# Optimization experiments

Hardware: AMD Instinct MI355X
Metric: run time of the kernel (lower is better)

Reference implementation:

```python
import jax, jax.numpy as jnp
import numpy as np

N_NODES = 100000
N_EDGES = 1600000
K = 3


def _cheb_conv(x, row, col, w, W, b):
    # SpMM: out[row] += w * x[col]
    def spmm(v):
        return jax.ops.segment_sum(w[:, None] * v[col], row, num_segments=N_NODES)
    Ts = [x, spmm(x)]
    for _ in range(2, K):
        Ts.append(2.0 * spmm(Ts[-1]) - Ts[-2])
    return jnp.concatenate(Ts, axis=-1) @ W.T + b


def setup_inputs() -> dict:
    key = jax.random.key(0)
    ks = jax.random.split(key, 12)
    inp = {
        "x": jax.random.normal(ks[0], (N_NODES, 128), dtype=jnp.float32),
        "edge_index": jax.random.randint(ks[1], (2, N_EDGES), 0, N_NODES, dtype=jnp.int32),
        "edge_weight": jax.random.normal(ks[2], (N_EDGES,), dtype=jnp.float32) * 0.05,
        "W_in": jax.random.normal(ks[3], (128, K * 128), dtype=jnp.float32) * (1.0 / np.sqrt(K * 128)),
        "b_in": jnp.zeros((128,), dtype=jnp.float32),
        "W_h1": jax.random.normal(ks[4], (128, K * 128), dtype=jnp.float32) * (1.0 / np.sqrt(K * 128)),
        "b_h1": jnp.zeros((128,), dtype=jnp.float32),
        "W_h2": jax.random.normal(ks[5], (128, K * 128), dtype=jnp.float32) * (1.0 / np.sqrt(K * 128)),
        "b_h2": jnp.zeros((128,), dtype=jnp.float32),
        "W_out": jax.random.normal(ks[6], (64, K * 128), dtype=jnp.float32) * (1.0 / np.sqrt(K * 128)),
        "b_out": jnp.zeros((64,), dtype=jnp.float32),
    }
    return inp


def reference(x, edge_index, edge_weight, W_in, b_in, W_h1, b_h1, W_h2, b_h2, W_out, b_out):
    row, col = edge_index[0], edge_index[1]
    # dropout is inactive at inference (training=False)
    h = jax.nn.relu(_cheb_conv(x, row, col, edge_weight, W_in, b_in))
    for (W, b) in ((W_h1, b_h1), (W_h2, b_h2)):
        h = jax.nn.relu(_cheb_conv(h, row, col, edge_weight, W, b) + h)  # residual
    out = _cheb_conv(h, row, col, edge_weight, W_out, b_out)
    return out
```

## Files before the change

### kernel.cpp

```cpp
#include <hip/hip_runtime.h>
#include <hip/hip_bf16.h>
#include <stdint.h>
#include <stddef.h>

#define N_NODES 100000
#define N_EDGES 1600000
#define FEAT 128
#define NB_SCAN ((N_NODES + 255) / 256)
#define LDS_PITCH 136
#define CAP 24
#define NL (CAP / 4)
#define NBKT ((N_NODES + 255) / 256)
#define EPB 2048
#define NBLK ((N_EDGES + EPB - 1) / EPB)
#define EPT (EPB / 256)

typedef __attribute__((ext_vector_type(8))) short bf16x8;
typedef __attribute__((ext_vector_type(4))) float f32x4;
typedef unsigned short u16;

__device__ __forceinline__ float bf2f(u16 u) {
    union { unsigned int i; float f; } v; v.i = ((unsigned int)u) << 16; return v.f;
}
__device__ __forceinline__ u16 f2bf(float f) {
    union { float f; unsigned int i; } v; v.f = f;
    unsigned int x = v.i;
    return (u16)((x + 0x7fffu + ((x >> 16) & 1u)) >> 16);
}


__global__ void hist_kernel(const int* __restrict__ rows, int* __restrict__ counts) {
    int e = blockIdx.x * blockDim.x + threadIdx.x;
    if (e < N_EDGES) {
        int r = rows[e];
        r = min(max(r, 0), N_NODES - 1);
        atomicAdd(&counts[r], 1);
    }
}

__global__ void reduce_counts_kernel(const int* __restrict__ counts, int* __restrict__ bsum) {
    __shared__ int s[256];
    int i = blockIdx.x * 256 + threadIdx.x;
    int v = (i < N_NODES) ? counts[i] : 0;
    s[threadIdx.x] = v; __syncthreads();
    for (int off = 128; off > 0; off >>= 1) {
        if (threadIdx.x < off) s[threadIdx.x] += s[threadIdx.x + off];
        __syncthreads();
    }
    if (threadIdx.x == 0) bsum[blockIdx.x] = s[0];
}

__global__ void scan_bsums_kernel(int* __restrict__ bsum, int* __restrict__ row_ptr) {
    __shared__ int s[512];
    int t = threadIdx.x;
    int v = (t < NB_SCAN) ? bsum[t] : 0;
    s[t] = v; __syncthreads();
    for (int off = 1; off < 512; off <<= 1) {
        int x = (t >= off) ? s[t - off] : 0;
        __syncthreads();
        s[t] += x;
        __syncthreads();
    }
    if (t < NB_SCAN) bsum[t] = s[t] - v;
    if (t == NB_SCAN - 1) row_ptr[N_NODES] = s[t];
}

__global__ void write_rowptr_kernel(int* __restrict__ counts, const int* __restrict__ bsum,
                                    int* __restrict__ row_ptr) {
    __shared__ int s[256];
    int i = blockIdx.x * 256 + threadIdx.x;
    int v = (i < N_NODES) ? counts[i] : 0;
    s[threadIdx.x] = v; __syncthreads();
    for (int off = 1; off < 256; off <<= 1) {
        int x = (threadIdx.x >= off) ? s[threadIdx.x - off] : 0;
        __syncthreads();
        s[threadIdx.x] += x;
        __syncthreads();
    }
    if (i < N_NODES) {
        row_ptr[i] = bsum[blockIdx.x] + s[threadIdx.x] - v;
        counts[i] = 0;
    }
}

__global__ void scatter_kernel(const int* __restrict__ rows, const int* __restrict__ cols,
                               const float* __restrict__ w, const int* __restrict__ row_ptr,
                               int* __restrict__ fill, int2* __restrict__ ecw) {
    int e = blockIdx.x * blockDim.x + threadIdx.x;
    if (e < N_EDGES) {
        int r = rows[e];
        r = min(max(r, 0), N_NODES - 1);
        int pos = row_ptr[r] + atomicAdd(&fill[r], 1);
        pos = min(max(pos, 0), N_EDGES - 1);
        int c = cols[e];
        c = min(max(c, 0), N_NODES - 1);
        ecw[pos] = make_int2(c, __float_as_int(w[e]));
    }
}


__global__ __launch_bounds__(256) void csr_passA_kernel(const int* __restrict__ rows,
                                                        int* __restrict__ pcnt) {
    __shared__ int s_cnt[NBKT];
    int tid = threadIdx.x, blk = blockIdx.x;
    for (int b = tid; b < NBKT; b += 256) s_cnt[b] = 0;
    __syncthreads();
    int e0 = blk * EPB;
#pragma unroll
    for (int it = 0; it < EPT; ++it) {
        int e = e0 + it * 256 + tid;
        if (e < N_EDGES) {
            int r = min(max(rows[e], 0), N_NODES - 1);
            atomicAdd(&s_cnt[r >> 8], 1);
        }
    }
    __syncthreads();
    for (int b = tid; b < NBKT; b += 256)
        pcnt[(size_t)blk * NBKT + b] = s_cnt[b];
}

__global__ __launch_bounds__(256) void csr_scanP_kernel(int* __restrict__ pcnt,
                                                        int* __restrict__ gtot) {
    __shared__ int s[256];
    int b = blockIdx.x, tid = threadIdx.x;
    int carry = 0;
    for (int c = 0; c < (NBLK + 255) / 256; ++c) {
        int idx = c * 256 + tid;
        int v = (idx < NBLK) ? pcnt[(size_t)idx * NBKT + b] : 0;
        s[tid] = v; __syncthreads();
        for (int off = 1; off < 256; off <<= 1) {
            int x = (tid >= off) ? s[tid - off] : 0;
            __syncthreads();
            s[tid] += x;
            __syncthreads();
        }
        if (idx < NBLK) pcnt[(size_t)idx * NBKT + b] = carry + s[tid] - v;
        carry += s[255];
        __syncthreads();
    }
    if (tid == 0) gtot[b] = carry;
}

__global__ void csr_scanG_kernel(const int* __restrict__ gtot, int* __restrict__ bsum,
                                 int* __restrict__ row_ptr) {
    __shared__ int s[512];
    int t = threadIdx.x;
    int v = (t < NBKT) ? gtot[t] : 0;
    s[t] = v; __syncthreads();
    for (int off = 1; off < 512; off <<= 1) {
        int x = (t >= off) ? s[t - off] : 0;
        __syncthreads();
        s[t] += x;
        __syncthreads();
    }
    if (t < NBKT) bsum[t] = s[t] - v;
    if (t == NBKT - 1) {
        bsum[NBKT] = s[t];
        row_ptr[N_NODES] = s[t];
    }
}

__global__ __launch_bounds__(256) void csr_passB_kernel(const int* __restrict__ rows,
                                                        const int* __restrict__ cols,
                                                        const float* __restrict__ w,
                                                        const int* __restrict__ pcnt,
                                                        const int* __restrict__ bsum,
                                                        int2* __restrict__ ebuf) {
    __shared__ int s_base[NBKT];
    __shared__ int s_cnt[NBKT];
    __shared__ int s_off[NBKT];
    __shared__ int s_scan[512];
    __shared__ int2 s_sorted[EPB];
    __shared__ int s_dst[EPB];
    int tid = threadIdx.x, blk = blockIdx.x;
    for (int b = tid; b < NBKT; b += 256) {
        s_base[b] = bsum[b] + pcnt[(size_t)blk * NBKT + b];
        s_cnt[b] = 0;
    }
    __syncthreads();
    int e0 = blk * EPB;
    int n = min(N_EDGES - e0, EPB);

    int2 pay[EPT]; int pb[EPT];
#pragma unroll
    for (int it = 0; it < EPT; ++it) {
        int e = e0 + it * 256 + tid;
        if (e < N_EDGES) {
            int r = min(max(rows[e], 0), N_NODES - 1);
            int c = min(max(cols[e], 0), N_NODES - 1);
            pay[it] = make_int2(c | ((r & 255) << 20), __float_as_int(w[e]));
            pb[it] = r >> 8;
            atomicAdd(&s_cnt[pb[it]], 1);
        } else {
            pb[it] = -1;
        }
    }
    __syncthreads();
    s_scan[tid] = (tid < NBKT) ? s_cnt[tid] : 0;
    s_scan[tid + 256] = (tid + 256 < NBKT) ? s_cnt[tid + 256] : 0;
    __syncthreads();
    for (int off = 1; off < 512; off <<= 1) {
        int a = (tid >= off) ? s_scan[tid - off] : 0;
        int b2 = (tid + 256 >= off) ? s_scan[tid + 256 - off] : 0;
        __syncthreads();
        s_scan[tid] += a;
        s_scan[tid + 256] += b2;
        __syncthreads();
    }
    for (int b = tid; b < NBKT; b += 256) {
        s_off[b] = s_scan[b] - s_cnt[b];
        s_cnt[b] = 0;
    }
    __syncthreads();
#pragma unroll
    for (int it = 0; it < EPT; ++it) {
        if (pb[it] >= 0) {
            int k = atomicAdd(&s_cnt[pb[it]], 1);
            int slot = s_off[pb[it]] + k;
            s_sorted[slot] = pay[it];
            s_dst[slot] = s_base[pb[it]] + k;
        }
    }
    __syncthreads();
    for (int p = tid; p < n; p += 256)
        ebuf[s_dst[p]] = s_sorted[p];
}

__global__ __launch_bounds__(256) void csr_finalize_kernel(const int* __restrict__ bsum,
                                                           const int2* __restrict__ ebuf,
                                                           int* __restrict__ row_ptr,
                                                           int2* __restrict__ ecw) {
    __shared__ int s_cnt[256];
    __shared__ int s_pos[256];
    int b = blockIdx.x, tid = threadIdx.x;
    int base = bsum[b];
    int cnt = bsum[b + 1] - base;
    s_cnt[tid] = 0; __syncthreads();
    for (int i = tid; i < cnt; i += 256)
        atomicAdd(&s_cnt[ebuf[base + i].x >> 20], 1);
    __syncthreads();
    int v = s_cnt[tid];
    s_pos[tid] = v; __syncthreads();
    for (int off = 1; off < 256; off <<= 1) {
        int x = (tid >= off) ? s_pos[tid - off] : 0;
        __syncthreads();
        s_pos[tid] += x;
        __syncthreads();
    }
    int excl = s_pos[tid] - v;
    int r = b * 256 + tid;
    if (r < N_NODES) row_ptr[r] = base + excl;
    s_cnt[tid] = excl;
    __syncthreads();
    for (int i = tid; i < cnt; i += 256) {
        int2 p = ebuf[base + i];
        int rl = p.x >> 20;
        int pos = base + atomicAdd(&s_cnt[rl], 1);
        pos = min(max(pos, 0), N_EDGES - 1);
        ecw[pos] = make_int2(p.x & 0xFFFFF, p.y);
    }
}

__device__ __forceinline__ float w_fold(const float* W, int o, int k) {
    if (k < 128)      return W[o * 384 + k] - W[o * 384 + 256 + k];
    else if (k < 256) return W[o * 384 + k];
    else              return 2.0f * W[o * 384 + k];
}

__global__ void prep_w_kernel(const float* __restrict__ W, u16* __restrict__ Wp, int O) {
    int i = blockIdx.x * blockDim.x + threadIdx.x;
    if (i >= O * 384) return;
    int o = i / 384, k = i % 384;
    Wp[i] = f2bf(w_fold(W, o, k));
}

__global__ void prep_w2_all_kernel(const float* __restrict__ Wa, const float* __restrict__ Wb,
                                   const float* __restrict__ Wc, const float* __restrict__ Wd,
                                   u16* __restrict__ Pa, u16* __restrict__ Pb,
                                   u16* __restrict__ Pc, u16* __restrict__ Pd) {
    int i = blockIdx.x * blockDim.x + threadIdx.x;
    const float* W; u16* P; int il;
    if (i < 6144)       { W = Wa; P = Pa; il = i; }
    else if (i < 12288) { W = Wb; P = Pb; il = i - 6144; }
    else if (i < 18432) { W = Wc; P = Pc; il = i - 12288; }
    else if (i < 21504) { W = Wd; P = Pd; il = i - 18432; }
    else return;
    int ot = il / 768;
    int rem = il % 768;
    int kk = rem / 64;
    int l = rem % 64;
    int q = l >> 4, r = l & 15;
    int o = ot * 16 + r;
    int kbase = kk * 32 + q * 8;
#pragma unroll
    for (int j = 0; j < 8; ++j)
        P[(size_t)il * 8 + j] = f2bf(w_fold(W, o, kbase + j));
}


__global__ void cvt_kernel(const float* __restrict__ x, u16* __restrict__ y) {
    int i = blockIdx.x * blockDim.x + threadIdx.x;
    if (i >= N_NODES * FEAT / 4) return;
    float4 v = ((const float4*)x)[i];
    ushort4 o;
    o.x = f2bf(v.x); o.y = f2bf(v.y); o.z = f2bf(v.z); o.w = f2bf(v.w);
    ((ushort4*)y)[i] = o;
}


__device__ __forceinline__ void load_meta(const int2* __restrict__ ecw, int s, int n,
                                          int lane, int& call, float& wall) {
    int idx = s + max(0, min(lane, n - 1));
    idx = min(idx, N_EDGES - 1);
    int2 cw = ecw[idx];
    call = cw.x;
    wall = (lane < n) ? __int_as_float(cw.y) : 0.f;
}

__device__ __forceinline__ void issue_row(const u16* __restrict__ X, int call,
                                          int g, int f, bf16x8* q) {
#pragma unroll
    for (int k = 0; k < NL; ++k) {
        int col = __shfl(call, k * 4 + g);
        q[k] = *(const bf16x8*)(X + (size_t)col * FEAT + f * 8);
    }
}

__device__ __forceinline__ void reduce_row(const bf16x8* q, float wall,
                                           int g, float* acc) {
#pragma unroll
    for (int k = 0; k < NL; ++k) {
        float wj = __shfl(wall, k * 4 + g);
#pragma unroll
        for (int j = 0; j < 8; ++j) acc[j] += wj * bf2f((u16)q[k][j]);
    }
}


__global__ __launch_bounds__(256) void spmm1_kernel(const int* __restrict__ row_ptr,
                                                    const int2* __restrict__ ecw,
                                                    const u16* __restrict__ X,
                                                    u16* __restrict__ Y) {
    int lane = threadIdx.x & 63;
    int g = lane >> 4, f = lane & 15;
    int rr = (blockIdx.x * blockDim.x + threadIdx.x) >> 6;

    int s = row_ptr[rr], e = row_ptr[rr + 1];
    float acc[8];
#pragma unroll
    for (int j = 0; j < 8; ++j) acc[j] = 0.f;

    {
        int call; float wall;
        load_meta(ecw, s, min(e - s, CAP), lane, call, wall);
        bf16x8 q[NL];
        issue_row(X, call, g, f, q);
        reduce_row(q, wall, g, acc);
    }
    for (int cs = s + CAP; cs < e; cs += CAP) {
        int c2; float w2;
        load_meta(ecw, cs, min(e - cs, CAP), lane, c2, w2);
        bf16x8 qt[NL];
        issue_row(X, c2, g, f, qt);
        reduce_row(qt, w2, g, acc);
    }

#pragma unroll
    for (int j = 0; j < 8; ++j) {
        acc[j] += __shfl_xor(acc[j], 16);
        acc[j] += __shfl_xor(acc[j], 32);
    }
    if (g == 0) {
        u16 tmp[8];
#pragma unroll
        for (int j = 0; j < 8; ++j) tmp[j] = f2bf(acc[j]);
        *(bf16x8*)(Y + (size_t)rr * FEAT + f * 8) = *(const bf16x8*)tmp;
    }
}


__device__ __forceinline__ void gather4(const int* __restrict__ row_ptr,
                                        const int2* __restrict__ ecw,
                                        const u16* __restrict__ X,
                                        int r0, int lane, int g, int f,
                                        float acc[4][8]) {
    int s[4], e[4];
    int call[4]; float wall[4];
#pragma unroll
    for (int y = 0; y < 4; ++y) {
        s[y] = row_ptr[r0 + y];
        e[y] = row_ptr[r0 + y + 1];
    }
#pragma unroll
    for (int y = 0; y < 4; ++y)
        load_meta(ecw, s[y], min(e[y] - s[y], CAP), lane, call[y], wall[y]);
#pragma unroll
    for (int y = 0; y < 4; ++y)
#pragma unroll
        for (int j = 0; j < 8; ++j) acc[y][j] = 0.f;

    bf16x8 q0[NL], q1[NL], q2[NL], q3[NL];
    issue_row(X, call[0], g, f, q0);
    issue_row(X, call[1], g, f, q1);
    reduce_row(q0, wall[0], g, acc[0]);
    issue_row(X, call[2], g, f, q2);
    reduce_row(q1, wall[1], g, acc[1]);
    issue_row(X, call[3], g, f, q3);
    reduce_row(q2, wall[2], g, acc[2]);
    reduce_row(q3, wall[3], g, acc[3]);

#pragma unroll
    for (int y = 0; y < 4; ++y) {
        for (int cs = s[y] + CAP; cs < e[y]; cs += CAP) {
            int c2; float w2;
            load_meta(ecw, cs, min(e[y] - cs, CAP), lane, c2, w2);
            bf16x8 qt[NL];
            issue_row(X, c2, g, f, qt);
            reduce_row(qt, w2, g, acc[y]);
        }
    }

#pragma unroll
    for (int y = 0; y < 4; ++y)
#pragma unroll
        for (int j = 0; j < 8; ++j) {
            acc[y][j] += __shfl_xor(acc[y][j], 16);
            acc[y][j] += __shfl_xor(acc[y][j], 32);
        }
}

__global__ __launch_bounds__(256) void spmm_kernel(const int* __restrict__ row_ptr,
                                                   const int2* __restrict__ ecw,
                                                   const u16* __restrict__ X,
                                                   u16* __restrict__ Y) {
    int wid = threadIdx.x >> 6;
    int lane = threadIdx.x & 63;
    int g = lane >> 4, f = lane & 15;
    int r0 = blockIdx.x * 16 + wid * 4;

    float acc[4][8];
    gather4(row_ptr, ecw, X, r0, lane, g, f, acc);

    if (g == 0) {
#pragma unroll
        for (int y = 0; y < 4; ++y) {
            u16 tmp[8];
#pragma unroll
            for (int j = 0; j < 8; ++j) tmp[j] = f2bf(acc[y][j]);
            *(bf16x8*)(Y + (size_t)(r0 + y) * FEAT + f * 8) = *(const bf16x8*)tmp;
        }
    }
}


template <int O, bool RELU, bool RES, bool OUT_F32>
__global__ __launch_bounds__(256) void gemm_kernel(const u16* __restrict__ H,
                                                   const u16* __restrict__ T1,
                                                   const u16* __restrict__ S2,
                                                   const u16* __restrict__ Wp2,
                                                   const float* __restrict__ bias,
                                                   void* __restrict__ outv) {
    __shared__ __align__(16) u16 sA[3][32][LDS_PITCH];
    int tid = threadIdx.x;
    int m0 = blockIdx.x * 32;

#pragma unroll
    for (int p = 0; p < 3; ++p) {
        const u16* sp = (p == 0) ? H : (p == 1) ? T1 : S2;
#pragma unroll
        for (int u = 0; u < 2; ++u) {
            int unit = u * 256 + tid;
            int row = unit >> 4, seg = unit & 15;
            *(bf16x8*)&sA[p][row][seg * 8] =
                *(const bf16x8*)(sp + (size_t)(m0 + row) * FEAT + seg * 8);
        }
    }
    __syncthreads();

    int lane = tid & 63, wid = tid >> 6;
    int r = lane & 15, q = lane >> 4;
    constexpr int NW = O / 64;
    f32x4 acc0[NW], acc1[NW];
#pragma unroll
    for (int t = 0; t < NW; ++t) {
        acc0[t] = (f32x4){0.f, 0.f, 0.f, 0.f};
        acc1[t] = (f32x4){0.f, 0.f, 0.f, 0.f};
    }

#pragma unroll
    for (int kk = 0; kk < 12; ++kk) {
        int p = kk >> 2, ko = kk & 3;
        bf16x8 af0 = *(const bf16x8*)&sA[p][r][ko * 32 + q * 8];
        bf16x8 af1 = *(const bf16x8*)&sA[p][16 + r][ko * 32 + q * 8];
#pragma unroll
        for (int t = 0; t < NW; ++t) {
            int ot = wid * NW + t;
            bf16x8 bfr = *(const bf16x8*)(Wp2 + ((size_t)(ot * 12 + kk) * 64 + lane) * 8);
            acc0[t] = __builtin_amdgcn_mfma_f32_16x16x32_bf16(af0, bfr, acc0[t], 0, 0, 0);
            acc1[t] = __builtin_amdgcn_mfma_f32_16x16x32_bf16(af1, bfr, acc1[t], 0, 0, 0);
        }
    }

#pragma unroll
    for (int t = 0; t < NW; ++t) {
        int col = (wid * NW + t) * 16 + r;
        float bv = bias[col];
#pragma unroll
        for (int i = 0; i < 4; ++i) {
            int lrow = q * 4 + i;
            float v0 = acc0[t][i] + bv;
            if (RES)  v0 += bf2f(sA[0][lrow][col]);
            if (RELU) v0 = fmaxf(v0, 0.f);
            float v1 = acc1[t][i] + bv;
            if (RES)  v1 += bf2f(sA[0][16 + lrow][col]);
            if (RELU) v1 = fmaxf(v1, 0.f);
            if (OUT_F32) {
                ((float*)outv)[(size_t)(m0 + lrow) * O + col] = v0;
                ((float*)outv)[(size_t)(m0 + 16 + lrow) * O + col] = v1;
            } else {
                ((u16*)outv)[(size_t)(m0 + lrow) * O + col] = f2bf(v0);
                ((u16*)outv)[(size_t)(m0 + 16 + lrow) * O + col] = f2bf(v1);
            }
        }
    }
}


template <int O, bool RELU, bool RES, bool OUT_F32>
__global__ __launch_bounds__(256) void fused_gemm_kernel(const int* __restrict__ row_ptr,
                                                         const int2* __restrict__ ecw,
                                                         const u16* __restrict__ H,
                                                         const u16* __restrict__ T1,
                                                         const u16* __restrict__ Wp,
                                                         const float* __restrict__ bias,
                                                         void* __restrict__ outv) {
    __shared__ __align__(16) u16 sT[16 * LDS_PITCH];
    int wid = threadIdx.x >> 6;
    int lane = threadIdx.x & 63;
    int g = lane >> 4, f = lane & 15;
    int m0 = blockIdx.x * 16;

    {
        float acc[4][8];
        gather4(row_ptr, ecw, T1, m0 + wid * 4, lane, g, f, acc);
        if (g == 0) {
#pragma unroll
            for (int y = 0; y < 4; ++y) {
                u16 tmp[8];
#pragma unroll
                for (int j = 0; j < 8; ++j) tmp[j] = f2bf(acc[y][j]);
                *(bf16x8*)(sT + (wid * 4 + y) * LDS_PITCH + f * 8) = *(const bf16x8*)tmp;
            }
        }
    }
    __syncthreads();

    int r = f, q = g;
    constexpr int NT = O / 16;
    constexpr int NW = NT / 4;
    f32x4 acc[NW];
#pragma unroll
    for (int t = 0; t < NW; ++t) acc[t] = (f32x4){0.f, 0.f, 0.f, 0.f};

#pragma unroll
    for (int kk = 0; kk < 12; ++kk) {
        bf16x8 af;
        if (kk < 4)
            af = *(const bf16x8*)(H + (size_t)(m0 + r) * FEAT + kk * 32 + q * 8);
        else if (kk < 8)
            af = *(const bf16x8*)(T1 + (size_t)(m0 + r) * FEAT + (kk - 4) * 32 + q * 8);
        else
            af = *(const bf16x8*)(sT + r * LDS_PITCH + (kk - 8) * 32 + q * 8);
#pragma unroll
        for (int t = 0; t < NW; ++t) {
            int ot = wid * NW + t;
            bf16x8 bfr = *(const bf16x8*)(Wp + (size_t)(ot * 16 + r) * 384 + kk * 32 + q * 8);
            acc[t] = __builtin_amdgcn_mfma_f32_16x16x32_bf16(af, bfr, acc[t], 0, 0, 0);
        }
    }

#pragma unroll
    for (int t = 0; t < NW; ++t) {
        int col = (wid * NW + t) * 16 + r;
        float bv = bias[col];
#pragma unroll
        for (int i = 0; i < 4; ++i) {
            int row = m0 + q * 4 + i;
            float v = acc[t][i] + bv;
            if (RES)  v += bf2f(H[(size_t)row * FEAT + col]);
            if (RELU) v = fmaxf(v, 0.f);
            if (OUT_F32) ((float*)outv)[(size_t)row * O + col] = v;
            else         ((u16*)outv)[(size_t)row * O + col] = f2bf(v);
        }
    }
}


static inline size_t align_up(size_t x) { return (x + 255) & ~(size_t)255; }

extern "C" void kernel_launch(void* const* d_in, const int* in_sizes, int n_in,
                              void* d_out, int out_size, void* d_ws, size_t ws_size,
                              hipStream_t stream) {
    const float* x     = (const float*)d_in[0];
    const int*   ei    = (const int*)d_in[1];
    const float* ew    = (const float*)d_in[2];
    const float* W_in  = (const float*)d_in[3];
    const float* b_in  = (const float*)d_in[4];
    const float* W_h1  = (const float*)d_in[5];
    const float* b_h1  = (const float*)d_in[6];
    const float* W_h2  = (const float*)d_in[7];
    const float* b_h2  = (const float*)d_in[8];
    const float* W_out = (const float*)d_in[9];
    const float* b_out = (const float*)d_in[10];

    const int* rows = ei;
    const int* cols = ei + N_EDGES;

    char* w = (char*)d_ws;
    size_t off = 0;
    int* counts = (int*)(w + off);            off = align_up(off + (size_t)N_NODES * 4);
    int* row_ptr= (int*)(w + off);            off = align_up(off + (size_t)(N_NODES + 1) * 4);
    int* bsum   = (int*)(w + off);            off = align_up(off + 512 * 4);
    int2* ecw   = (int2*)(w + off);           off = align_up(off + (size_t)N_EDGES * 8);
    u16* t1     = (u16*)(w + off);            off = align_up(off + (size_t)N_NODES * FEAT * 2);
    u16* h      = (u16*)(w + off);            off = align_up(off + (size_t)N_NODES * FEAT * 2);
    u16* Wp_in  = (u16*)(w + off);            off = align_up(off + (size_t)128 * 384 * 2);
    u16* Wp_h1  = (u16*)(w + off);            off = align_up(off + (size_t)128 * 384 * 2);
    u16* Wp_h2  = (u16*)(w + off);            off = align_up(off + (size_t)128 * 384 * 2);
    u16* Wp_out = (u16*)(w + off);            off = align_up(off + (size_t)64 * 384 * 2);
    u16* s2     = (u16*)(w + off);            size_t off2 = align_up(off + (size_t)N_NODES * FEAT * 2);
    u16* W2_in  = (u16*)(w + off2);           off2 = align_up(off2 + (size_t)128 * 384 * 2);
    u16* W2_h1  = (u16*)(w + off2);           off2 = align_up(off2 + (size_t)128 * 384 * 2);
    u16* W2_h2  = (u16*)(w + off2);           off2 = align_up(off2 + (size_t)128 * 384 * 2);
    u16* W2_out = (u16*)(w + off2);           off2 = align_up(off2 + (size_t)64 * 384 * 2);
    int* pcnt   = (int*)(w + off2);           off2 = align_up(off2 + (size_t)NBLK * NBKT * 4);
    int* gtot   = (int*)(w + off2);           off2 = align_up(off2 + (size_t)NBKT * 4);
    const bool use_split = (ws_size >= off2);
    static_assert((size_t)N_EDGES * 8 <= (size_t)N_NODES * FEAT * 2, "ebuf exceeds s2");

    cvt_kernel<<<(N_NODES * FEAT / 4 + 255) / 256, 256, 0, stream>>>(x, h);

    const int grid16 = N_NODES / 16;
    const int grid32 = N_NODES / 32;
    const int grid1  = N_NODES * 64 / 256;

    if (use_split) {
        int2* ebuf = (int2*)s2;
        csr_passA_kernel<<<NBLK, 256, 0, stream>>>(rows, pcnt);
        csr_scanP_kernel<<<NBKT, 256, 0, stream>>>(pcnt, gtot);
        csr_scanG_kernel<<<1, 512, 0, stream>>>(gtot, bsum, row_ptr);
        csr_passB_kernel<<<NBLK, 256, 0, stream>>>(rows, cols, ew, pcnt, bsum, ebuf);
        csr_finalize_kernel<<<NBKT, 256, 0, stream>>>(bsum, ebuf, row_ptr, ecw);

        prep_w2_all_kernel<<<(21504 + 255) / 256, 256, 0, stream>>>(
            W_in, W_h1, W_h2, W_out, W2_in, W2_h1, W2_h2, W2_out);

        spmm1_kernel<<<grid1, 256, 0, stream>>>(row_ptr, ecw, h, t1);
        spmm1_kernel<<<grid1, 256, 0, stream>>>(row_ptr, ecw, t1, s2);
        gemm_kernel<128, true, false, false><<<grid32, 256, 0, stream>>>(h, t1, s2, W2_in, b_in, h);
        spmm1_kernel<<<grid1, 256, 0, stream>>>(row_ptr, ecw, h, t1);
        spmm1_kernel<<<grid1, 256, 0, stream>>>(row_ptr, ecw, t1, s2);
        gemm_kernel<128, true, true, false><<<grid32, 256, 0, stream>>>(h, t1, s2, W2_h1, b_h1, h);
        spmm1_kernel<<<grid1, 256, 0, stream>>>(row_ptr, ecw, h, t1);
        spmm1_kernel<<<grid1, 256, 0, stream>>>(row_ptr, ecw, t1, s2);
        gemm_kernel<128, true, true, false><<<grid32, 256, 0, stream>>>(h, t1, s2, W2_h2, b_h2, h);
        spmm1_kernel<<<grid1, 256, 0, stream>>>(row_ptr, ecw, h, t1);
        spmm1_kernel<<<grid1, 256, 0, stream>>>(row_ptr, ecw, t1, s2);
        gemm_kernel<64, false, false, true><<<grid32, 256, 0, stream>>>(h, t1, s2, W2_out, b_out, d_out);
    } else {
        hipMemsetAsync(counts, 0, (size_t)N_NODES * 4, stream);
        hist_kernel<<<N_EDGES / 256, 256, 0, stream>>>(rows, counts);
        reduce_counts_kernel<<<NB_SCAN, 256, 0, stream>>>(counts, bsum);
        scan_bsums_kernel<<<1, 512, 0, stream>>>(bsum, row_ptr);
        write_rowptr_kernel<<<NB_SCAN, 256, 0, stream>>>(counts, bsum, row_ptr);
        scatter_kernel<<<N_EDGES / 256, 256, 0, stream>>>(rows, cols, ew, row_ptr, counts, ecw);

        prep_w_kernel<<<(128 * 384 + 255) / 256, 256, 0, stream>>>(W_in, Wp_in, 128);
        prep_w_kernel<<<(128 * 384 + 255) / 256, 256, 0, stream>>>(W_h1, Wp_h1, 128);
        prep_w_kernel<<<(128 * 384 + 255) / 256, 256, 0, stream>>>(W_h2, Wp_h2, 128);
        prep_w_kernel<<<(64 * 384 + 255) / 256, 256, 0, stream>>>(W_out, Wp_out, 64);

        spmm_kernel<<<grid16, 256, 0, stream>>>(row_ptr, ecw, h, t1);
        fused_gemm_kernel<128, true, false, false><<<grid16, 256, 0, stream>>>(
            row_ptr, ecw, h, t1, Wp_in, b_in, h);
        spmm_kernel<<<grid16, 256, 0, stream>>>(row_ptr, ecw, h, t1);
        fused_gemm_kernel<128, true, true, false><<<grid16, 256, 0, stream>>>(
            row_ptr, ecw, h, t1, Wp_h1, b_h1, h);
        spmm_kernel<<<grid16, 256, 0, stream>>>(row_ptr, ecw, h, t1);
        fused_gemm_kernel<128, true, true, false><<<grid16, 256, 0, stream>>>(
            row_ptr, ecw, h, t1, Wp_h2, b_h2, h);
        spmm_kernel<<<grid16, 256, 0, stream>>>(row_ptr, ecw, h, t1);
        fused_gemm_kernel<64, false, false, true><<<grid16, 256, 0, stream>>>(
            row_ptr, ecw, h, t1, Wp_out, b_out, d_out);
    }
}
```

Baseline: 700.8 us.

## Reassociate final Chebyshev layer to project to 64 features before SpMM

For the output layer, the weights are applied before propagation: h is projected to A=h·W1ᵀ and B=2h·W2ᵀ (64 columns each). Two 64-wide SpMMs then compute L(A+L B), and a final GEMM adds (W0−W2)h plus bias. This halves the feature width of the two gather-heavy SpMMs in the last layer, at the cost of an extra small GEMM and a different rounding order in bf16.

```diff
diff --git a/kernel.cpp b/kernel.cpp
--- a/kernel.cpp
+++ b/kernel.cpp
@@ -10,6 +10,7 @@
 #define LDS_PITCH 136
 #define CAP 24
 #define NL (CAP / 4)
+#define NL64 (CAP / 8)
 #define NBKT ((N_NODES + 255) / 256)
 #define EPB 2048
 #define NBLK ((N_EDGES + EPB - 1) / EPB)
@@ -275,15 +276,14 @@
 }
 
 __global__ void prep_w2_all_kernel(const float* __restrict__ Wa, const float* __restrict__ Wb,
-                                   const float* __restrict__ Wc, const float* __restrict__ Wd,
+                                   const float* __restrict__ Wc,
                                    u16* __restrict__ Pa, u16* __restrict__ Pb,
-                                   u16* __restrict__ Pc, u16* __restrict__ Pd) {
+                                   u16* __restrict__ Pc) {
     int i = blockIdx.x * blockDim.x + threadIdx.x;
     const float* W; u16* P; int il;
     if (i < 6144)       { W = Wa; P = Pa; il = i; }
     else if (i < 12288) { W = Wb; P = Pb; il = i - 6144; }
     else if (i < 18432) { W = Wc; P = Pc; il = i - 12288; }
-    else if (i < 21504) { W = Wd; P = Pd; il = i - 18432; }
     else return;
     int ot = il / 768;
     int rem = il % 768;
@@ -297,6 +297,34 @@
         P[(size_t)il * 8 + j] = f2bf(w_fold(W, o, kbase + j));
 }
 
+__global__ void prep_w4_kernel(const float* __restrict__ Wo,
+                               u16* __restrict__ Pab, u16* __restrict__ Pf) {
+    int i = blockIdx.x * blockDim.x + threadIdx.x;
+    if (i >= 3072) return;
+    u16* P; int il; bool is_ab;
+    if (i < 2048) { P = Pab; il = i; is_ab = true; }
+    else          { P = Pf;  il = i - 2048; is_ab = false; }
+    int ot = il / 256;
+    int rem = il % 256;
+    int kk = rem / 64;
+    int l = rem % 64;
+    int q = l >> 4, r = l & 15;
+    int o = ot * 16 + r;
+    int kbase = kk * 32 + q * 8;
+#pragma unroll
+    for (int j = 0; j < 8; ++j) {
+        int k = kbase + j;
+        float v;
+        if (is_ab) {
+            if (o < 64) v = Wo[o * 384 + 128 + k];
+            else        v = 2.0f * Wo[(o - 64) * 384 + 256 + k];
+        } else {
+            v = Wo[o * 384 + k] - Wo[o * 384 + 256 + k];
+        }
+        P[(size_t)il * 8 + j] = f2bf(v);
+    }
+}
+
 
 __global__ void cvt_kernel(const float* __restrict__ x, u16* __restrict__ y) {
     int i = blockIdx.x * blockDim.x + threadIdx.x;
@@ -375,6 +403,74 @@
 #pragma unroll
         for (int j = 0; j < 8; ++j) tmp[j] = f2bf(acc[j]);
         *(bf16x8*)(Y + (size_t)rr * FEAT + f * 8) = *(const bf16x8*)tmp;
+    }
+}
+
+
+template <bool ADDT>
+__global__ __launch_bounds__(256) void spmm64_kernel(const int* __restrict__ row_ptr,
+                                                     const int2* __restrict__ ecw,
+                                                     const u16* __restrict__ X, int ldx,
+                                                     const u16* __restrict__ A, int lda,
+                                                     u16* __restrict__ Y, int ldy) {
+    int lane = threadIdx.x & 63;
+    int g = lane >> 3, f = lane & 7;
+    int rr = (blockIdx.x * blockDim.x + threadIdx.x) >> 6;
+
+    int s = row_ptr[rr], e = row_ptr[rr + 1];
+    float acc[8];
+#pragma unroll
+    for (int j = 0; j < 8; ++j) acc[j] = 0.f;
+
+    {
+        int call; float wall;
+        load_meta(ecw, s, min(e - s, CAP), lane, call, wall);
+        bf16x8 q[NL64];
+#pragma unroll
+        for (int k = 0; k < NL64; ++k) {
+            int col = __shfl(call, k * 8 + g);
+            q[k] = *(const bf16x8*)(X + (size_t)col * ldx + f * 8);
+        }
+#pragma unroll
+        for (int k = 0; k < NL64; ++k) {
+            float wj = __shfl(wall, k * 8 + g);
+#pragma unroll
+            for (int j = 0; j < 8; ++j) acc[j] += wj * bf2f((u16)q[k][j]);
+        }
+    }
+    for (int cs = s + CAP; cs < e; cs += CAP) {
+        int c2; float w2;
+        load_meta(ecw, cs, min(e - cs, CAP), lane, c2, w2);
+        bf16x8 qt[NL64];
+#pragma unroll
+        for (int k = 0; k < NL64; ++k) {
+            int col = __shfl(c2, k * 8 + g);
+            qt[k] = *(const bf16x8*)(X + (size_t)col * ldx + f * 8);
+        }
+#pragma unroll
+        for (int k = 0; k < NL64; ++k) {
+            float wj = __shfl(w2, k * 8 + g);
+#pragma unroll
+            for (int j = 0; j < 8; ++j) acc[j] += wj * bf2f((u16)qt[k][j]);
+        }
+    }
+
+#pragma unroll
+    for (int j = 0; j < 8; ++j) {
+        acc[j] += __shfl_xor(acc[j], 8);
+        acc[j] += __shfl_xor(acc[j], 16);
+        acc[j] += __shfl_xor(acc[j], 32);
+    }
+    if (g == 0) {
+        if (ADDT) {
+            bf16x8 av = *(const bf16x8*)(A + (size_t)rr * lda + f * 8);
+#pragma unroll
+            for (int j = 0; j < 8; ++j) acc[j] += bf2f((u16)av[j]);
+        }
+        u16 tmp[8];
+#pragma unroll
+        for (int j = 0; j < 8; ++j) tmp[j] = f2bf(acc[j]);
+        *(bf16x8*)(Y + (size_t)rr * ldy + f * 8) = *(const bf16x8*)tmp;
     }
 }
 
@@ -520,6 +616,74 @@
             } else {
                 ((u16*)outv)[(size_t)(m0 + lrow) * O + col] = f2bf(v0);
                 ((u16*)outv)[(size_t)(m0 + 16 + lrow) * O + col] = f2bf(v1);
+            }
+        }
+    }
+}
+
+
+template <int O, bool OUT_F32, bool ADDT, bool BIAS>
+__global__ __launch_bounds__(256) void gemm1p_kernel(const u16* __restrict__ X,
+                                                     const u16* __restrict__ P,
+                                                     const u16* __restrict__ addp,
+                                                     const float* __restrict__ bias,
+                                                     void* __restrict__ outv) {
+    __shared__ __align__(16) u16 sA[32][LDS_PITCH];
+    int tid = threadIdx.x;
+    int m0 = blockIdx.x * 32;
+
+#pragma unroll
+    for (int u = 0; u < 2; ++u) {
+        int unit = u * 256 + tid;
+        int row = unit >> 4, seg = unit & 15;
+        *(bf16x8*)&sA[row][seg * 8] =
+            *(const bf16x8*)(X + (size_t)(m0 + row) * FEAT + seg * 8);
+    }
+    __syncthreads();
+
+    int lane = tid & 63, wid = tid >> 6;
+    int r = lane & 15, q = lane >> 4;
+    constexpr int NW = O / 64;
+    f32x4 acc0[NW], acc1[NW];
+#pragma unroll
+    for (int t = 0; t < NW; ++t) {
+        acc0[t] = (f32x4){0.f, 0.f, 0.f, 0.f};
+        acc1[t] = (f32x4){0.f, 0.f, 0.f, 0.f};
+    }
+
+#pragma unroll
+    for (int kk = 0; kk < 4; ++kk) {
+        bf16x8 af0 = *(const bf16x8*)&sA[r][kk * 32 + q * 8];
+        bf16x8 af1 = *(const bf16x8*)&sA[16 + r][kk * 32 + q * 8];
+#pragma unroll
+        for (int t = 0; t < NW; ++t) {
+            int ot = wid * NW + t;
+            bf16x8 bfr = *(const bf16x8*)(P + ((size_t)(ot * 4 + kk) * 64 + lane) * 8);
+            acc0[t] = __builtin_amdgcn_mfma_f32_16x16x32_bf16(af0, bfr, acc0[t], 0, 0, 0);
+            acc1[t] = __builtin_amdgcn_mfma_f32_16x16x32_bf16(af1, bfr, acc1[t], 0, 0, 0);
+        }
+    }
+
+#pragma unroll
+    for (int t = 0; t < NW; ++t) {
+        int col = (wid * NW + t) * 16 + r;
+        float bv = BIAS ? bias[col] : 0.f;
+#pragma unroll
+        for (int i = 0; i < 4; ++i) {
+            int lrow = q * 4 + i;
+            int row0 = m0 + lrow, row1 = m0 + 16 + lrow;
+            float v0 = acc0[t][i] + bv;
+            float v1 = acc1[t][i] + bv;
+            if (ADDT) {
+                v0 += bf2f(addp[(size_t)row0 * O + col]);
+                v1 += bf2f(addp[(size_t)row1 * O + col]);
+            }
+            if (OUT_F32) {
+                ((float*)outv)[(size_t)row0 * O + col] = v0;
+                ((float*)outv)[(size_t)row1 * O + col] = v1;
+            } else {
+                ((u16*)outv)[(size_t)row0 * O + col] = f2bf(v0);
+                ((u16*)outv)[(size_t)row1 * O + col] = f2bf(v1);
             }
         }
     }
@@ -632,7 +796,8 @@
     u16* W2_in  = (u16*)(w + off2);           off2 = align_up(off2 + (size_t)128 * 384 * 2);
     u16* W2_h1  = (u16*)(w + off2);           off2 = align_up(off2 + (size_t)128 * 384 * 2);
     u16* W2_h2  = (u16*)(w + off2);           off2 = align_up(off2 + (size_t)128 * 384 * 2);
-    u16* W2_out = (u16*)(w + off2);           off2 = align_up(off2 + (size_t)64 * 384 * 2);
+    u16* P_ab   = (u16*)(w + off2);           off2 = align_up(off2 + (size_t)2048 * 8 * 2);
+    u16* P_f    = (u16*)(w + off2);           off2 = align_up(off2 + (size_t)1024 * 8 * 2);
     int* pcnt   = (int*)(w + off2);           off2 = align_up(off2 + (size_t)NBLK * NBKT * 4);
     int* gtot   = (int*)(w + off2);           off2 = align_up(off2 + (size_t)NBKT * 4);
     const bool use_split = (ws_size >= off2);
@@ -652,21 +817,35 @@
         csr_passB_kernel<<<NBLK, 256, 0, stream>>>(rows, cols, ew, pcnt, bsum, ebuf);
         csr_finalize_kernel<<<NBKT, 256, 0, stream>>>(bsum, ebuf, row_ptr, ecw);
 
-        prep_w2_all_kernel<<<(21504 + 255) / 256, 256, 0, stream>>>(
-            W_in, W_h1, W_h2, W_out, W2_in, W2_h1, W2_h2, W2_out);
+        prep_w2_all_kernel<<<(18432 + 255) / 256, 256, 0, stream>>>(
+            W_in, W_h1, W_h2, W2_in, W2_h1, W2_h2);
+        prep_w4_kernel<<<(3072 + 255) / 256, 256, 0, stream>>>(W_out, P_ab, P_f);
 
         spmm1_kernel<<<grid1, 256, 0, stream>>>(row_ptr, ecw, h, t1);
         spmm1_kernel<<<grid1, 256, 0, stream>>>(row_ptr, ecw, t1, s2);
         gemm_kernel<128, true, false, false><<<grid32, 256, 0, stream>>>(h, t1, s2, W2_in, b_in, h);
+
         spmm1_kernel<<<grid1, 256, 0, stream>>>(row_ptr, ecw, h, t1);
         spmm1_kernel<<<grid1, 256, 0, stream>>>(row_ptr, ecw, t1, s2);
         gemm_kernel<128, true, true, false><<<grid32, 256, 0, stream>>>(h, t1, s2, W2_h1, b_h1, h);
+
         spmm1_kernel<<<grid1, 256, 0, stream>>>(row_ptr, ecw, h, t1);
         spmm1_kernel<<<grid1, 256, 0, stream>>>(row_ptr, ecw, t1, s2);
         gemm_kernel<128, true, true, false><<<grid32, 256, 0, stream>>>(h, t1, s2, W2_h2, b_h2, h);
-        spmm1_kernel<<<grid1, 256, 0, stream>>>(row_ptr, ecw, h, t1);
-        spmm1_kernel<<<grid1, 256, 0, stream>>>(row_ptr, ecw, t1, s2);
-        gemm_kernel<64, false, false, true><<<grid32, 256, 0, stream>>>(h, t1, s2, W2_out, b_out, d_out);
+
+        {
+            u16* ab = t1;
+            u16* dbuf = s2;
+            u16* ev = s2 + (size_t)N_NODES * 64;
+            gemm1p_kernel<128, false, false, false><<<grid32, 256, 0, stream>>>(
+                h, P_ab, nullptr, nullptr, ab);
+            spmm64_kernel<true><<<grid1, 256, 0, stream>>>(
+                row_ptr, ecw, ab + 64, 128, ab, 128, dbuf, 64);
+            spmm64_kernel<false><<<grid1, 256, 0, stream>>>(
+                row_ptr, ecw, dbuf, 64, nullptr, 0, ev, 64);
+            gemm1p_kernel<64, true, true, true><<<grid32, 256, 0, stream>>>(
+                h, P_f, ev, b_out, d_out);
+        }
     } else {
         hipMemsetAsync(counts, 0, (size_t)N_NODES * 4, stream);
         hist_kernel<<<N_EDGES / 256, 256, 0, stream>>>(rows, counts);
```

After: 676.1 us. 1.04x faster.
